# Performance work log

Measured on AMD Instinct MI355X. Metric: run time of the kernel, lower is better.

Reference implementation:

```python
import jax, jax.numpy as jnp
import numpy as np

VOCAB, HID, L, HEADS, INTER, MAXSEQ, NCLS = 30522, 128, 2, 2, 512, 512, 2
HEAD = HID // HEADS
B, S = 128, 512


def _tlin(x, W, b):
    # TernaryLinear: threshold-quantize W to {-1,0,1} with per-tensor scale,
    # then ordinary linear. delta = 0.7*mean|W|, alpha = mean|W| over kept entries.
    absW = jnp.abs(W)
    delta = 0.7 * jnp.mean(absW)
    mask = (absW > delta).astype(W.dtype)
    alpha = jnp.sum(absW * mask) / jnp.maximum(jnp.sum(mask), 1.0)
    Wq = jnp.sign(W) * mask * alpha  # [out, in]
    return jnp.einsum('...i,oi->...o', x, Wq) + b


def _ln(x, g, b, eps=1e-5):
    m = jnp.mean(x, axis=-1, keepdims=True)
    v = jnp.var(x, axis=-1, keepdims=True)
    return (x - m) * jax.lax.rsqrt(v + eps) * g + b


def setup_inputs() -> dict:
    key = jax.random.key(0)
    ks = iter(jax.random.split(key, 64))
    n = lambda shape, s=0.02: jax.random.normal(next(ks), shape, dtype=jnp.float32) * s
    inp = {
        'input_ids': jax.random.randint(next(ks), (B, S), 0, VOCAB, dtype=jnp.int32).astype(jnp.int64),
        'tok_emb': n((VOCAB, HID)),
        'pos_emb': n((MAXSEQ, HID)),
        'ln_g': jnp.ones((HID,), jnp.float32), 'ln_b': jnp.zeros((HID,), jnp.float32),
        'qw': n((L, HID, HID)), 'qb': jnp.zeros((L, HID), jnp.float32),
        'kw': n((L, HID, HID)), 'kb': jnp.zeros((L, HID), jnp.float32),
        'vw': n((L, HID, HID)), 'vb': jnp.zeros((L, HID), jnp.float32),
        'aow': n((L, HID, HID)), 'aob': jnp.zeros((L, HID), jnp.float32),
        'iw': n((L, INTER, HID)), 'ib': jnp.zeros((L, INTER), jnp.float32),
        'fow': n((L, HID, INTER)), 'fob': jnp.zeros((L, HID), jnp.float32),
        'ln1g': jnp.ones((L, HID), jnp.float32), 'ln1b': jnp.zeros((L, HID), jnp.float32),
        'ln2g': jnp.ones((L, HID), jnp.float32), 'ln2b': jnp.zeros((L, HID), jnp.float32),
        'clf_w': n((NCLS, HID)), 'clf_b': jnp.zeros((NCLS,), jnp.float32),
    }
    return inp


def reference(input_ids, tok_emb, pos_emb, ln_g, ln_b, qw, qb, kw, kb, vw, vb,
              aow, aob, iw, ib, fow, fob, ln1g, ln1b, ln2g, ln2b, clf_w, clf_b):
    b, s = input_ids.shape
    x = tok_emb[input_ids] + pos_emb[jnp.arange(s)][None, :, :]  # [B,S,H]
    x = _ln(x, ln_g, ln_b)
    scale = 1.0 / (HEAD ** 0.5)
    for l in range(L):
        q = _tlin(x, qw[l], qb[l]).reshape(b, s, HEADS, HEAD)
        k = _tlin(x, kw[l], kb[l]).reshape(b, s, HEADS, HEAD)
        v = _tlin(x, vw[l], vb[l]).reshape(b, s, HEADS, HEAD)
        scores = jnp.einsum('bqhd,bkhd->bhqk', q, k) * scale
        attn = jax.nn.softmax(scores, axis=-1)
        ctx = jnp.einsum('bhqk,bkhd->bqhd', attn, v).reshape(b, s, HID)
        attn_out = _tlin(ctx, aow[l], aob[l])
        x = _ln(x + attn_out, ln1g[l], ln1b[l])
        ff = _tlin(jax.nn.relu(_tlin(x, iw[l], ib[l])), fow[l], fob[l])
        x = _ln(x + ff, ln2g[l], ln2b[l])
    cls = x[:, 0, :]
    logits = _tlin(cls, clf_w, clf_b)  # [B, NCLS]
    return logits
```

## Files before the change

kernel.cpp:

```cpp
#include <hip/hip_runtime.h>

typedef short bf8s __attribute__((ext_vector_type(8)));
typedef float f32x4 __attribute__((ext_vector_type(4)));

#define MFMA16(a, b, c) __builtin_amdgcn_mfma_f32_16x16x32_bf16(a, b, c, 0, 0, 0)

constexpr int S_ = 512, HID_ = 128, B_ = 128, M_ = B_ * S_;

__device__ inline short f2bf(float f) {
  unsigned u = __float_as_uint(f);
  u = (u + 0x7fffu + ((u >> 16) & 1u)) >> 16;
  return (short)u;
}
__device__ inline float bf2f(short s) {
  return __uint_as_float(((unsigned)(unsigned short)s) << 16);
}

__device__ inline float block_red1024(float v, float* red) {
  #pragma unroll
  for (int m = 32; m >= 1; m >>= 1) v += __shfl_xor(v, m);
  __syncthreads();
  if ((threadIdx.x & 63) == 0) red[threadIdx.x >> 6] = v;
  __syncthreads();
  float t = 0.f;
  #pragma unroll
  for (int i = 0; i < 16; ++i) t += red[i];
  return t;
}

__device__ inline void mat_info(int mat, const float* qw, const float* kw,
                                const float* vw, const float* aow, const float* iw,
                                const float* fw, const float* cw,
                                const float** src, int* n, int* doff) {
  if (mat < 6) {
    int l = mat / 3, which = mat % 3;
    const float* t[3] = {qw, kw, vw};
    *src = t[which] + l * 16384; *n = 16384; *doff = l * 49152 + which * 16384;
  } else if (mat < 8) {
    int l = mat - 6;
    *src = aow + l * 16384; *n = 16384; *doff = 98304 + l * 16384;
  } else if (mat < 10) {
    *src = iw + (mat - 8) * 65536; *n = 65536; *doff = 131072 + (mat - 8) * 65536;
  } else if (mat < 12) {
    *src = fw + (mat - 10) * 65536; *n = 65536; *doff = 262144 + (mat - 10) * 65536;
  } else {
    *src = cw; *n = 256; *doff = 393216;
  }
}

__global__ __launch_bounds__(1024) void k_qe(const float* qw, const float* kw,
    const float* vw, const float* aow, const float* iw, const float* fw,
    const float* cw, short* WQ,
    const int* __restrict__ ids, const float* __restrict__ tok,
    const float* __restrict__ pos, const float* __restrict__ g,
    const float* __restrict__ bb, short* xb) {
  __shared__ float red[16];
  int tid = threadIdx.x;
  if (blockIdx.x < 13) {
    const float* src; int n, doff;
    mat_info(blockIdx.x, qw, kw, vw, aow, iw, fw, cw, &src, &n, &doff);
    float s = 0.f;
    for (int i = tid; i < n; i += 1024) s += fabsf(src[i]);
    s = block_red1024(s, red);
    float delta = 0.7f * s / (float)n;
    float s2 = 0.f, c2 = 0.f;
    for (int i = tid; i < n; i += 1024) {
      float a = fabsf(src[i]);
      if (a > delta) { s2 += a; c2 += 1.f; }
    }
    s2 = block_red1024(s2, red);
    c2 = block_red1024(c2, red);
    float alpha = s2 / fmaxf(c2, 1.f);
    for (int i = tid; i < n; i += 1024) {
      float w = src[i];
      WQ[doff + i] = (fabsf(w) > delta) ? f2bf(w > 0.f ? alpha : -alpha) : (short)0;
    }
  } else {
    int wave = tid >> 6, lane = tid & 63;
    int t = (blockIdx.x - 13) * 16 + wave;
    int s = t & (S_ - 1);
    int id = ids[t];
    float e0 = tok[(size_t)id * HID_ + lane] + pos[(size_t)s * HID_ + lane];
    float e1 = tok[(size_t)id * HID_ + 64 + lane] + pos[(size_t)s * HID_ + 64 + lane];
    float sum = e0 + e1, ssq = e0 * e0 + e1 * e1;
    #pragma unroll
    for (int m = 32; m >= 1; m >>= 1) {
      sum += __shfl_xor(sum, m);
      ssq += __shfl_xor(ssq, m);
    }
    float mean = sum / 128.f;
    float var = ssq / 128.f - mean * mean;
    float rs = rsqrtf(var + 1e-5f);
    size_t o = (size_t)t * HID_;
    xb[o + lane]      = f2bf((e0 - mean) * rs * g[lane] + bb[lane]);
    xb[o + 64 + lane] = f2bf((e1 - mean) * rs * g[64 + lane] + bb[64 + lane]);
  }
}

__global__ __launch_bounds__(256) void k_qkv(
    const short* __restrict__ A, const short* __restrict__ W,
    const float* __restrict__ b0, const float* __restrict__ b1,
    const float* __restrict__ b2, short* outb) {
  __shared__ short Wl[128 * 144];
  int tid = threadIdx.x, lane = tid & 63, wave = tid >> 6;
  int row16 = lane & 15, quad = lane >> 4;
  int tok0 = blockIdx.x * 64 + wave * 16;
  int nbase = blockIdx.y * 128;

  const short* arow = A + (size_t)(tok0 + row16) * 128 + quad * 8;
  bf8s av[4];
  #pragma unroll
  for (int ki = 0; ki < 4; ++ki) av[ki] = *(const bf8s*)(arow + ki * 32);

  {
    int r = tid >> 1, half = tid & 1;
    const short* src = W + (size_t)(nbase + r) * 128 + half * 64;
    short* dst = &Wl[r * 144 + half * 64];
    #pragma unroll
    for (int j = 0; j < 8; ++j)
      *(bf8s*)(dst + j * 8) = *(const bf8s*)(src + j * 8);
  }
  __syncthreads();

  f32x4 acc[8] = {};
  #pragma unroll
  for (int ki = 0; ki < 4; ++ki)
    #pragma unroll
    for (int ot = 0; ot < 8; ++ot) {
      bf8s b = *(const bf8s*)(&Wl[(ot * 16 + row16) * 144 + ki * 32 + quad * 8]);
      acc[ot] = MFMA16(av[ki], b, acc[ot]);
    }

  const float* bp = (blockIdx.y == 0) ? b0 : ((blockIdx.y == 1) ? b1 : b2);
  float osc = (blockIdx.y == 0) ? 0.125f : 1.0f;
  int m0 = tok0 + quad * 4;
  #pragma unroll
  for (int ot = 0; ot < 8; ++ot) {
    int col = ot * 16 + row16;
    float bi = bp[col];
    #pragma unroll
    for (int r = 0; r < 4; ++r) {
      float v = (acc[ot][r] + bi) * osc;
      outb[(size_t)(m0 + r) * 384 + nbase + col] = f2bf(v);
    }
  }
}

template <int DOQKV>
__global__ __launch_bounds__(512, 2) void k_aoff(
    const short* __restrict__ cb, const short* __restrict__ Wa,
    const float* __restrict__ aob, const float* __restrict__ ln1g,
    const float* __restrict__ ln1b, const short* __restrict__ Wi,
    const short* __restrict__ Wf, const float* __restrict__ ib,
    const float* __restrict__ fb, const float* __restrict__ ln2g,
    const float* __restrict__ ln2b, short* xb,
    const short* __restrict__ Wqkv2, const float* __restrict__ qb2,
    const float* __restrict__ kb2, const float* __restrict__ vb2,
    short* qkvout) {
  __shared__ short SM[29696];
  int tid = threadIdx.x, lane = tid & 63, wave = tid >> 6;
  int row16 = lane & 15, quad = lane >> 4;
  int tok0 = blockIdx.x * 128 + wave * 16;
  int m0 = tok0 + quad * 4;

  const short* arow = cb + (size_t)(tok0 + row16) * 128 + quad * 8;
  bf8s av[4];
  #pragma unroll
  for (int ki = 0; ki < 4; ++ki) av[ki] = *(const bf8s*)(arow + ki * 32);

  {
    int r = tid >> 2, q4 = tid & 3;
    const short* src = Wa + (size_t)r * 128 + q4 * 32;
    short* dst = &SM[r * 144 + q4 * 32];
    #pragma unroll
    for (int j = 0; j < 4; ++j)
      *(bf8s*)(dst + j * 8) = *(const bf8s*)(src + j * 8);
  }
  __syncthreads();

  f32x4 acc[8] = {};
  #pragma unroll
  for (int ki = 0; ki < 4; ++ki)
    #pragma unroll
    for (int ot = 0; ot < 8; ++ot) {
      bf8s b = *(const bf8s*)(&SM[(ot * 16 + row16) * 144 + ki * 32 + quad * 8]);
      acc[ot] = MFMA16(av[ki], b, acc[ot]);
    }

  {
    float sum[4] = {}, ssq[4] = {};
    #pragma unroll
    for (int ot = 0; ot < 8; ++ot) {
      int col = ot * 16 + row16;
      float bi = aob[col];
      #pragma unroll
      for (int r = 0; r < 4; ++r) {
        float v = acc[ot][r] + bi + bf2f(xb[(size_t)(m0 + r) * HID_ + col]);
        acc[ot][r] = v;
        sum[r] += v; ssq[r] += v * v;
      }
    }
    #pragma unroll
    for (int m = 1; m <= 8; m <<= 1)
      #pragma unroll
      for (int r = 0; r < 4; ++r) {
        sum[r] += __shfl_xor(sum[r], m);
        ssq[r] += __shfl_xor(ssq[r], m);
      }
    float mean[4], rstd[4];
    #pragma unroll
    for (int r = 0; r < 4; ++r) {
      mean[r] = sum[r] / 128.f;
      float var = ssq[r] / 128.f - mean[r] * mean[r];
      rstd[r] = rsqrtf(var + 1e-5f);
    }
    #pragma unroll
    for (int ot = 0; ot < 8; ++ot) {
      int col = ot * 16 + row16;
      float gg = ln1g[col], bb2 = ln1b[col];
      #pragma unroll
      for (int r = 0; r < 4; ++r)
        acc[ot][r] = (acc[ot][r] - mean[r]) * rstd[r] * gg + bb2;
    }
  }

  #pragma unroll
  for (int ot = 0; ot < 8; ++ot) {
    int col = ot * 16 + row16;
    #pragma unroll
    for (int r = 0; r < 4; ++r)
      xb[(size_t)(m0 + r) * HID_ + col] = f2bf(acc[ot][r]);
  }

  __syncthreads();
  {
    short* myX = &SM[wave * 2304];
    #pragma unroll
    for (int ot = 0; ot < 8; ++ot)
      #pragma unroll
      for (int r = 0; r < 4; ++r)
        myX[(quad * 4 + r) * 144 + ot * 16 + row16] = f2bf(acc[ot][r]);
    #pragma unroll
    for (int ki = 0; ki < 4; ++ki)
      av[ki] = *(const bf8s*)(myX + row16 * 144 + ki * 32 + quad * 8);
  }

  int rwi = tid >> 3, q8 = tid & 7;
  int rwf = tid >> 2, qf4 = tid & 3;
  short* SWi = SM;
  short* SWf = SM + 9216;
  short* mySt = SM + 19456 + wave * 1280;
  f32x4 acc2[8] = {};
  for (int c = 0; c < 8; ++c) {
    __syncthreads();
    {
      const short* ws1 = Wi + (size_t)(c * 64 + rwi) * HID_ + q8 * 16;
      const short* ws2 = Wf + (size_t)rwf * 512 + c * 64 + qf4 * 16;
      bf8s a0 = *(const bf8s*)(ws1);
      bf8s a1 = *(const bf8s*)(ws1 + 8);
      bf8s b0 = *(const bf8s*)(ws2);
      bf8s b1 = *(const bf8s*)(ws2 + 8);
      short* dwi = SWi + rwi * 144 + q8 * 16;
      short* dwf = SWf + rwf * 80 + qf4 * 16;
      *(bf8s*)(dwi) = a0; *(bf8s*)(dwi + 8) = a1;
      *(bf8s*)(dwf) = b0; *(bf8s*)(dwf + 8) = b1;
    }
    __syncthreads();

    #pragma unroll
    for (int ot = 0; ot < 4; ++ot) {
      f32x4 hacc = {};
      #pragma unroll
      for (int ki = 0; ki < 4; ++ki) {
        bf8s b = *(const bf8s*)(SWi + (ot * 16 + row16) * 144 + ki * 32 + quad * 8);
        hacc = MFMA16(av[ki], b, hacc);
      }
      float bi = ib[c * 64 + ot * 16 + row16];
      #pragma unroll
      for (int r = 0; r < 4; ++r)
        mySt[(quad * 4 + r) * 80 + ot * 16 + row16] =
            f2bf(fmaxf(hacc[r] + bi, 0.f));
    }
    bf8s ha0 = *(const bf8s*)(mySt + row16 * 80 + quad * 8);
    bf8s ha1 = *(const bf8s*)(mySt + row16 * 80 + 32 + quad * 8);
    #pragma unroll
    for (int ot = 0; ot < 8; ++ot) {
      bf8s bA = *(const bf8s*)(SWf + (ot * 16 + row16) * 80 + quad * 8);
      bf8s bB = *(const bf8s*)(SWf + (ot * 16 + row16) * 80 + 32 + quad * 8);
      acc2[ot] = MFMA16(ha0, bA, acc2[ot]);
      acc2[ot] = MFMA16(ha1, bB, acc2[ot]);
    }
  }

  {
    float sum[4] = {}, ssq[4] = {};
    #pragma unroll
    for (int ot = 0; ot < 8; ++ot) {
      int col = ot * 16 + row16;
      float bi = fb[col];
      #pragma unroll
      for (int r = 0; r < 4; ++r) {
        float v = acc2[ot][r] + bi + bf2f(xb[(size_t)(m0 + r) * HID_ + col]);
        acc2[ot][r] = v;
        sum[r] += v; ssq[r] += v * v;
      }
    }
    #pragma unroll
    for (int m = 1; m <= 8; m <<= 1)
      #pragma unroll
      for (int r = 0; r < 4; ++r) {
        sum[r] += __shfl_xor(sum[r], m);
        ssq[r] += __shfl_xor(ssq[r], m);
      }
    float mean[4], rstd[4];
    #pragma unroll
    for (int r = 0; r < 4; ++r) {
      mean[r] = sum[r] / 128.f;
      float var = ssq[r] / 128.f - mean[r] * mean[r];
      rstd[r] = rsqrtf(var + 1e-5f);
    }
    #pragma unroll
    for (int ot = 0; ot < 8; ++ot) {
      int col = ot * 16 + row16;
      float gg = ln2g[col], bb2 = ln2b[col];
      #pragma unroll
      for (int r = 0; r < 4; ++r) {
        float v = (acc2[ot][r] - mean[r]) * rstd[r] * gg + bb2;
        acc2[ot][r] = v;
        xb[(size_t)(m0 + r) * HID_ + col] = f2bf(v);
      }
    }
  }

  if (DOQKV) {
    __syncthreads();
    bf8s av2[4];
    {
      short* myX = &SM[wave * 2304];
      #pragma unroll
      for (int ot = 0; ot < 8; ++ot)
        #pragma unroll
        for (int r = 0; r < 4; ++r)
          myX[(quad * 4 + r) * 144 + ot * 16 + row16] = f2bf(acc2[ot][r]);
      #pragma unroll
      for (int ki = 0; ki < 4; ++ki)
        av2[ki] = *(const bf8s*)(myX + row16 * 144 + ki * 32 + quad * 8);
    }
    for (int c3 = 0; c3 < 3; ++c3) {
      __syncthreads();
      {
        int r = tid >> 2, q4 = tid & 3;
        const short* src = Wqkv2 + (size_t)(c3 * 128 + r) * 128 + q4 * 32;
        short* dst = &SM[r * 144 + q4 * 32];
        #pragma unroll
        for (int j = 0; j < 4; ++j)
          *(bf8s*)(dst + j * 8) = *(const bf8s*)(src + j * 8);
      }
      __syncthreads();
      f32x4 acc3[8] = {};
      #pragma unroll
      for (int ki = 0; ki < 4; ++ki)
        #pragma unroll
        for (int ot = 0; ot < 8; ++ot) {
          bf8s b = *(const bf8s*)(&SM[(ot * 16 + row16) * 144 + ki * 32 + quad * 8]);
          acc3[ot] = MFMA16(av2[ki], b, acc3[ot]);
        }
      const float* bp = (c3 == 0) ? qb2 : ((c3 == 1) ? kb2 : vb2);
      float osc = (c3 == 0) ? 0.125f : 1.0f;
      #pragma unroll
      for (int ot = 0; ot < 8; ++ot) {
        int col = ot * 16 + row16;
        float bi = bp[col];
        #pragma unroll
        for (int r = 0; r < 4; ++r) {
          float v = (acc3[ot][r] + bi) * osc;
          qkvout[(size_t)(m0 + r) * 384 + c3 * 128 + col] = f2bf(v);
        }
      }
    }
  }
}

__global__ __launch_bounds__(512) void k_attn(const short* __restrict__ qkv,
                                              short* __restrict__ O) {
  __shared__ short Kl[64 * 72];
  __shared__ short Vtl[64 * 72];
  __shared__ short Pl[8][16 * 72];

  int tid = threadIdx.x, lane = tid & 63, wave = tid >> 6;
  int row16 = lane & 15, quad = lane >> 4;
  int b = blockIdx.x >> 2, h = (blockIdx.x >> 1) & 1, qhalf = blockIdx.x & 1;
  const short* base  = qkv + (size_t)b * S_ * 384;
  const short* kbase = base + 128 + h * 64;
  const short* vbase = base + 256 + h * 64;
  int q0 = qhalf * 256 + wave * 32;

  bf8s qa[2][2];
  #pragma unroll
  for (int qf = 0; qf < 2; ++qf) {
    const short* qrow = base + h * 64 +
        (size_t)(q0 + qf * 16 + row16) * 384 + quad * 8;
    qa[qf][0] = *(const bf8s*)(qrow);
    qa[qf][1] = *(const bf8s*)(qrow + 32);
  }

  int krow = tid >> 3, dgk = tid & 7;
  int vkey = tid & 63, dgv = tid >> 6;
  const short* kptr = kbase + (size_t)krow * 384 + dgk * 8;
  const short* vptr = vbase + (size_t)vkey * 384 + dgv * 8;
  bf8s kst = *(const bf8s*)(kptr);
  bf8s vst = *(const bf8s*)(vptr);

  float li[2][4] = {};
  f32x4 oacc[2][4] = {};
  short* myP = &Pl[wave][0];

  for (int kt0 = 0; kt0 < S_; kt0 += 64) {
    if (kt0) __syncthreads();
    *(bf8s*)(&Kl[krow * 72 + dgk * 8]) = kst;
    #pragma unroll
    for (int j = 0; j < 8; ++j) Vtl[(dgv * 8 + j) * 72 + vkey] = vst[j];
    __syncthreads();
    if (kt0 + 64 < S_) {
      kst = *(const bf8s*)(kptr + (size_t)(kt0 + 64) * 384);
      vst = *(const bf8s*)(vptr + (size_t)(kt0 + 64) * 384);
    }

    f32x4 sc[2][4] = {};
    #pragma unroll
    for (int ks = 0; ks < 4; ++ks) {
      const short* kp = &Kl[(ks * 16 + row16) * 72 + quad * 8];
      bf8s k0 = *(const bf8s*)(kp);
      bf8s k1 = *(const bf8s*)(kp + 32);
      sc[0][ks] = MFMA16(qa[0][0], k0, sc[0][ks]);
      sc[0][ks] = MFMA16(qa[0][1], k1, sc[0][ks]);
      sc[1][ks] = MFMA16(qa[1][0], k0, sc[1][ks]);
      sc[1][ks] = MFMA16(qa[1][1], k1, sc[1][ks]);
    }

    #pragma unroll
    for (int qf = 0; qf < 2; ++qf) {
      #pragma unroll
      for (int ks = 0; ks < 4; ++ks)
        #pragma unroll
        for (int r = 0; r < 4; ++r) {
          float pv = __expf(sc[qf][ks][r]);
          li[qf][r] += pv;
          myP[(quad * 4 + r) * 72 + ks * 16 + row16] = f2bf(pv);
        }
      bf8s pa0 = *(const bf8s*)(&myP[row16 * 72 + quad * 8]);
      bf8s pa1 = *(const bf8s*)(&myP[row16 * 72 + 32 + quad * 8]);
      #pragma unroll
      for (int dt = 0; dt < 4; ++dt) {
        const short* vp = &Vtl[(dt * 16 + row16) * 72 + quad * 8];
        bf8s v0 = *(const bf8s*)(vp);
        bf8s v1 = *(const bf8s*)(vp + 32);
        oacc[qf][dt] = MFMA16(pa0, v0, oacc[qf][dt]);
        oacc[qf][dt] = MFMA16(pa1, v1, oacc[qf][dt]);
      }
    }
  }

  #pragma unroll
  for (int qf = 0; qf < 2; ++qf) {
    float inv[4];
    #pragma unroll
    for (int r = 0; r < 4; ++r) {
      float t = li[qf][r];
      #pragma unroll
      for (int m = 1; m <= 8; m <<= 1) t += __shfl_xor(t, m);
      inv[r] = 1.f / t;
    }
    size_t trow = (size_t)(b * S_ + q0 + qf * 16 + quad * 4);
    #pragma unroll
    for (int dt = 0; dt < 4; ++dt)
      #pragma unroll
      for (int r = 0; r < 4; ++r)
        O[(trow + r) * HID_ + h * 64 + dt * 16 + row16] =
            f2bf(oacc[qf][dt][r] * inv[r]);
  }
}

__global__ __launch_bounds__(256) void k_clf(const short* __restrict__ xb,
    const short* __restrict__ Wc, const float* __restrict__ cbias, float* out) {
  int i = threadIdx.x;
  int b = i >> 1, c = i & 1;
  float s = 0.f;
  for (int k = 0; k < HID_; ++k)
    s += bf2f(xb[(size_t)b * S_ * HID_ + k]) * bf2f(Wc[c * HID_ + k]);
  out[b * 2 + c] = s + cbias[c];
}

extern "C" void kernel_launch(void* const* d_in, const int* in_sizes, int n_in,
                              void* d_out, int out_size, void* d_ws, size_t ws_size,
                              hipStream_t stream) {
  const int*   ids     = (const int*)d_in[0];
  const float* tok_emb = (const float*)d_in[1];
  const float* pos_emb = (const float*)d_in[2];
  const float* ln_g    = (const float*)d_in[3];
  const float* ln_bb   = (const float*)d_in[4];
  const float* qw      = (const float*)d_in[5];
  const float* qbias   = (const float*)d_in[6];
  const float* kw      = (const float*)d_in[7];
  const float* kbias   = (const float*)d_in[8];
  const float* vw      = (const float*)d_in[9];
  const float* vbias   = (const float*)d_in[10];
  const float* aow     = (const float*)d_in[11];
  const float* aobias  = (const float*)d_in[12];
  const float* iw      = (const float*)d_in[13];
  const float* ibias   = (const float*)d_in[14];
  const float* fow     = (const float*)d_in[15];
  const float* fbias   = (const float*)d_in[16];
  const float* ln1g    = (const float*)d_in[17];
  const float* ln1b    = (const float*)d_in[18];
  const float* ln2g    = (const float*)d_in[19];
  const float* ln2b    = (const float*)d_in[20];
  const float* clfw    = (const float*)d_in[21];
  const float* clfb    = (const float*)d_in[22];

  char* ws = (char*)d_ws;
  short* WQ  = (short*)ws;
  short* xb  = (short*)(ws + 1048576);
  short* qkv = (short*)(ws + 1048576 + 16777216);
  short* cb_ = qkv + (size_t)M_ * 384;

  k_qe<<<13 + M_ / 16, 1024, 0, stream>>>(qw, kw, vw, aow, iw, fow, clfw, WQ,
                                          ids, tok_emb, pos_emb, ln_g, ln_bb, xb);

  const short* Wqkv0 = WQ;
  const short* Wqkv1 = WQ + 49152;
  const short* Wa0   = WQ + 98304;
  const short* Wa1   = WQ + 98304 + 16384;
  const short* Wi0   = WQ + 131072;
  const short* Wi1   = WQ + 131072 + 65536;
  const short* Wf0   = WQ + 262144;
  const short* Wf1   = WQ + 262144 + 65536;

  k_qkv<<<dim3(M_ / 64, 3), 256, 0, stream>>>(
      xb, Wqkv0, qbias, kbias, vbias, qkv);
  k_attn<<<512, 512, 0, stream>>>(qkv, cb_);
  k_aoff<1><<<M_ / 128, 512, 0, stream>>>(
      cb_, Wa0, aobias, ln1g, ln1b, Wi0, Wf0, ibias, fbias, ln2g, ln2b, xb,
      Wqkv1, qbias + HID_, kbias + HID_, vbias + HID_, qkv);
  k_attn<<<512, 512, 0, stream>>>(qkv, cb_);
  k_aoff<0><<<M_ / 128, 512, 0, stream>>>(
      cb_, Wa1, aobias + HID_, ln1g + HID_, ln1b + HID_, Wi1, Wf1,
      ibias + 512, fbias + HID_, ln2g + HID_, ln2b + HID_, xb,
      nullptr, nullptr, nullptr, nullptr, nullptr);

  k_clf<<<1, 256, 0, stream>>>(xb, WQ + 393216, clfb, (float*)d_out);
}
```

Baseline: 319.1 us.

## Split attention into quarter-query blocks and fold log2e into Q scale

The attention grid doubles to 1024 blocks, each covering 128 queries, so each wave now handles 16 query rows instead of 32. This raises parallelism and cuts per-wave register use. The cost is that K/V tiles are loaded into LDS twice as often in total. The Q scale now includes log2(e), which lets the softmax use exp2f instead of __expf.

Result: slower. 340.4 us (+6.7%).

```diff
diff --git a/kernel.cpp b/kernel.cpp
--- a/kernel.cpp
+++ b/kernel.cpp
@@ -6,6 +6,7 @@
 #define MFMA16(a, b, c) __builtin_amdgcn_mfma_f32_16x16x32_bf16(a, b, c, 0, 0, 0)
 
 constexpr int S_ = 512, HID_ = 128, B_ = 128, M_ = B_ * S_;
+constexpr float QSC_ = 0.18033688f;
 
 __device__ inline short f2bf(float f) {
   unsigned u = __float_as_uint(f);
@@ -132,7 +133,7 @@
     }
 
   const float* bp = (blockIdx.y == 0) ? b0 : ((blockIdx.y == 1) ? b1 : b2);
-  float osc = (blockIdx.y == 0) ? 0.125f : 1.0f;
+  float osc = (blockIdx.y == 0) ? QSC_ : 1.0f;
   int m0 = tok0 + quad * 4;
   #pragma unroll
   for (int ot = 0; ot < 8; ++ot) {
@@ -366,7 +367,7 @@
           acc3[ot] = MFMA16(av2[ki], b, acc3[ot]);
         }
       const float* bp = (c3 == 0) ? qb2 : ((c3 == 1) ? kb2 : vb2);
-      float osc = (c3 == 0) ? 0.125f : 1.0f;
+      float osc = (c3 == 0) ? QSC_ : 1.0f;
       #pragma unroll
       for (int ot = 0; ot < 8; ++ot) {
         int col = ot * 16 + row16;
@@ -389,20 +390,15 @@
 
   int tid = threadIdx.x, lane = tid & 63, wave = tid >> 6;
   int row16 = lane & 15, quad = lane >> 4;
-  int b = blockIdx.x >> 2, h = (blockIdx.x >> 1) & 1, qhalf = blockIdx.x & 1;
+  int b = blockIdx.x >> 3, h = (blockIdx.x >> 2) & 1, qq = blockIdx.x & 3;
   const short* base  = qkv + (size_t)b * S_ * 384;
   const short* kbase = base + 128 + h * 64;
   const short* vbase = base + 256 + h * 64;
-  int q0 = qhalf * 256 + wave * 32;
-
-  bf8s qa[2][2];
-  #pragma unroll
-  for (int qf = 0; qf < 2; ++qf) {
-    const short* qrow = base + h * 64 +
-        (size_t)(q0 + qf * 16 + row16) * 384 + quad * 8;
-    qa[qf][0] = *(const bf8s*)(qrow);
-    qa[qf][1] = *(const bf8s*)(qrow + 32);
-  }
+  int q0 = qq * 128 + wave * 16;
+
+  const short* qrow = base + h * 64 + (size_t)(q0 + row16) * 384 + quad * 8;
+  bf8s qa0 = *(const bf8s*)(qrow);
+  bf8s qa1 = *(const bf8s*)(qrow + 32);
 
   int krow = tid >> 3, dgk = tid & 7;
   int vkey = tid & 63, dgv = tid >> 6;
@@ -411,8 +407,8 @@
   bf8s kst = *(const bf8s*)(kptr);
   bf8s vst = *(const bf8s*)(vptr);
 
-  float li[2][4] = {};
-  f32x4 oacc[2][4] = {};
+  float li[4] = {};
+  f32x4 oacc[4] = {};
   short* myP = &Pl[wave][0];
 
   for (int kt0 = 0; kt0 < S_; kt0 += 64) {
@@ -426,59 +422,51 @@
       vst = *(const bf8s*)(vptr + (size_t)(kt0 + 64) * 384);
     }
 
-    f32x4 sc[2][4] = {};
+    f32x4 sc[4] = {};
     #pragma unroll
     for (int ks = 0; ks < 4; ++ks) {
       const short* kp = &Kl[(ks * 16 + row16) * 72 + quad * 8];
       bf8s k0 = *(const bf8s*)(kp);
       bf8s k1 = *(const bf8s*)(kp + 32);
-      sc[0][ks] = MFMA16(qa[0][0], k0, sc[0][ks]);
-      sc[0][ks] = MFMA16(qa[0][1], k1, sc[0][ks]);
-      sc[1][ks] = MFMA16(qa[1][0], k0, sc[1][ks]);
-      sc[1][ks] = MFMA16(qa[1][1], k1, sc[1][ks]);
-    }
-
-    #pragma unroll
-    for (int qf = 0; qf < 2; ++qf) {
-      #pragma unroll
-      for (int ks = 0; ks < 4; ++ks)
-        #pragma unroll
-        for (int r = 0; r < 4; ++r) {
-          float pv = __expf(sc[qf][ks][r]);
-          li[qf][r] += pv;
-          myP[(quad * 4 + r) * 72 + ks * 16 + row16] = f2bf(pv);
-        }
-      bf8s pa0 = *(const bf8s*)(&myP[row16 * 72 + quad * 8]);
-      bf8s pa1 = *(const bf8s*)(&myP[row16 * 72 + 32 + quad * 8]);
-      #pragma unroll
-      for (int dt = 0; dt < 4; ++dt) {
-        const short* vp = &Vtl[(dt * 16 + row16) * 72 + quad * 8];
-        bf8s v0 = *(const bf8s*)(vp);
-        bf8s v1 = *(const bf8s*)(vp + 32);
-        oacc[qf][dt] = MFMA16(pa0, v0, oacc[qf][dt]);
-        oacc[qf][dt] = MFMA16(pa1, v1, oacc[qf][dt]);
-      }
-    }
-  }
-
-  #pragma unroll
-  for (int qf = 0; qf < 2; ++qf) {
-    float inv[4];
-    #pragma unroll
-    for (int r = 0; r < 4; ++r) {
-      float t = li[qf][r];
-      #pragma unroll
-      for (int m = 1; m <= 8; m <<= 1) t += __shfl_xor(t, m);
-      inv[r] = 1.f / t;
-    }
-    size_t trow = (size_t)(b * S_ + q0 + qf * 16 + quad * 4);
-    #pragma unroll
-    for (int dt = 0; dt < 4; ++dt)
-      #pragma unroll
-      for (int r = 0; r < 4; ++r)
-        O[(trow + r) * HID_ + h * 64 + dt * 16 + row16] =
-            f2bf(oacc[qf][dt][r] * inv[r]);
-  }
+      sc[ks] = MFMA16(qa0, k0, sc[ks]);
+      sc[ks] = MFMA16(qa1, k1, sc[ks]);
+    }
+
+    #pragma unroll
+    for (int ks = 0; ks < 4; ++ks)
+      #pragma unroll
+      for (int r = 0; r < 4; ++r) {
+        float pv = exp2f(sc[ks][r]);
+        li[r] += pv;
+        myP[(quad * 4 + r) * 72 + ks * 16 + row16] = f2bf(pv);
+      }
+    bf8s pa0 = *(const bf8s*)(&myP[row16 * 72 + quad * 8]);
+    bf8s pa1 = *(const bf8s*)(&myP[row16 * 72 + 32 + quad * 8]);
+    #pragma unroll
+    for (int dt = 0; dt < 4; ++dt) {
+      const short* vp = &Vtl[(dt * 16 + row16) * 72 + quad * 8];
+      bf8s v0 = *(const bf8s*)(vp);
+      bf8s v1 = *(const bf8s*)(vp + 32);
+      oacc[dt] = MFMA16(pa0, v0, oacc[dt]);
+      oacc[dt] = MFMA16(pa1, v1, oacc[dt]);
+    }
+  }
+
+  float inv[4];
+  #pragma unroll
+  for (int r = 0; r < 4; ++r) {
+    float t = li[r];
+    #pragma unroll
+    for (int m = 1; m <= 8; m <<= 1) t += __shfl_xor(t, m);
+    inv[r] = 1.f / t;
+  }
+  size_t trow = (size_t)(b * S_ + q0 + quad * 4);
+  #pragma unroll
+  for (int dt = 0; dt < 4; ++dt)
+    #pragma unroll
+    for (int r = 0; r < 4; ++r)
+      O[(trow + r) * HID_ + h * 64 + dt * 16 + row16] =
+          f2bf(oacc[dt][r] * inv[r]);
 }
 
 __global__ __launch_bounds__(256) void k_clf(const short* __restrict__ xb,
@@ -538,11 +526,11 @@
 
   k_qkv<<<dim3(M_ / 64, 3), 256, 0, stream>>>(
       xb, Wqkv0, qbias, kbias, vbias, qkv);
-  k_attn<<<512, 512, 0, stream>>>(qkv, cb_);
+  k_attn<<<1024, 512, 0, stream>>>(qkv, cb_);
   k_aoff<1><<<M_ / 128, 512, 0, stream>>>(
       cb_, Wa0, aobias, ln1g, ln1b, Wi0, Wf0, ibias, fbias, ln2g, ln2b, xb,
       Wqkv1, qbias + HID_, kbias + HID_, vbias + HID_, qkv);
-  k_attn<<<512, 512, 0, stream>>>(qkv, cb_);
+  k_attn<<<1024, 512, 0, stream>>>(qkv, cb_);
   k_aoff<0><<<M_ / 128, 512, 0, stream>>>(
       cb_, Wa1, aobias + HID_, ln1g + HID_, ln1b + HID_, Wi1, Wf1,
       ibias + 512, fbias + HID_, ln2g + HID_, ln2b + HID_, xb,
```
